# Kernel optimization log

Measured on AMD Instinct MI355X. Metric: run time of the kernel, lower is better.

## Reference

```python
import jax, jax.numpy as jnp
import numpy as np

# ---- static config (mirrors ProposalLayerModule param) ----
FEAT_STRIDE = 16
PRE_NMS_TOPN = 6000
POST_NMS_TOPN = 300
NMS_THRESH = 0.7
MIN_SIZE = 16.0
NUM_ANCHORS = 9


def _generate_anchors():
    """Replicates generate_anchors(base_size=16, ratios=[0.5,1,2], scales=[8,16,32])."""
    base = np.array([0.0, 0.0, 15.0, 15.0])
    ratios = np.array([0.5, 1.0, 2.0])
    scales = np.array([8.0, 16.0, 32.0])
    w = base[2] - base[0] + 1.0
    h = base[3] - base[1] + 1.0
    xc = base[0] + 0.5 * (w - 1.0)
    yc = base[1] + 0.5 * (h - 1.0)
    size = w * h
    ws = np.round(np.sqrt(size / ratios))
    hs = np.round(ws * ratios)
    ratio_anchors = np.stack([xc - 0.5 * (ws - 1), yc - 0.5 * (hs - 1),
                              xc + 0.5 * (ws - 1), yc + 0.5 * (hs - 1)], axis=1)
    out = []
    for a in ratio_anchors:
        aw = a[2] - a[0] + 1.0
        ah = a[3] - a[1] + 1.0
        axc = a[0] + 0.5 * (aw - 1.0)
        ayc = a[1] + 0.5 * (ah - 1.0)
        ws2 = aw * scales
        hs2 = ah * scales
        out.append(np.stack([axc - 0.5 * (ws2 - 1), ayc - 0.5 * (hs2 - 1),
                             axc + 0.5 * (ws2 - 1), ayc + 0.5 * (hs2 - 1)], axis=1))
    return np.concatenate(out, axis=0).astype(np.float32)  # (9, 4)

_ANCHORS = _generate_anchors()


def _nms_keep(iou, valid, thresh):
    """Greedy NMS over score-sorted boxes. Returns boolean keep mask."""
    n = iou.shape[0]
    idx = jnp.arange(n)
    def body(i, keep):
        sup = keep[i] & (iou[i] > thresh) & (idx > i)
        return keep & jnp.logical_not(sup)
    return jax.lax.fori_loop(0, n, body, valid)


def setup_inputs() -> dict:
    key = jax.random.key(0)
    k1, k2 = jax.random.split(key)
    H, W = 128, 192
    scores = jax.random.normal(k1, (1, 2 * NUM_ANCHORS, H, W), dtype=jnp.float32)
    # small deltas so exp(dw), exp(dh) stay in a realistic range
    bbox_deltas = jax.random.normal(k2, (1, 4 * NUM_ANCHORS, H, W), dtype=jnp.float32) * 0.1
    im_info = jnp.array([H * FEAT_STRIDE, W * FEAT_STRIDE, 1.0], dtype=jnp.float32)
    return {"scores": scores, "bbox_deltas": bbox_deltas, "im_info": im_info}


def reference(scores, bbox_deltas, im_info):
    A = NUM_ANCHORS
    s = scores[0, A:]                      # (A, H, W) fg scores
    Hf, Wf = s.shape[1], s.shape[2]
    # shifts, matching torch.meshgrid default indexing='ij' (x-major flatten)
    shift_x = jnp.arange(Wf, dtype=jnp.float32) * FEAT_STRIDE
    shift_y = jnp.arange(Hf, dtype=jnp.float32) * FEAT_STRIDE
    sx, sy = jnp.meshgrid(shift_x, shift_y, indexing='ij')   # (W, H)
    shifts = jnp.stack([sx.ravel(), sy.ravel(), sx.ravel(), sy.ravel()], axis=1)  # (K,4)
    anchors = (jnp.asarray(_ANCHORS)[None, :, :] + shifts[:, None, :]).reshape(-1, 4)  # (K*A,4)

    deltas = jnp.transpose(bbox_deltas[0], (1, 2, 0)).reshape(-1, 4)  # (H*W*A,4)
    sc = jnp.transpose(s, (1, 2, 0)).reshape(-1)                      # (H*W*A,)

    # bbox_transform_inv
    widths = anchors[:, 2] - anchors[:, 0] + 1.0
    heights = anchors[:, 3] - anchors[:, 1] + 1.0
    ctr_x = anchors[:, 0] + 0.5 * widths
    ctr_y = anchors[:, 1] + 0.5 * heights
    dx, dy, dw, dh = deltas[:, 0], deltas[:, 1], deltas[:, 2], deltas[:, 3]
    pcx = dx * widths + ctr_x
    pcy = dy * heights + ctr_y
    pw = jnp.exp(dw) * widths
    ph = jnp.exp(dh) * heights
    x1 = pcx - 0.5 * pw
    y1 = pcy - 0.5 * ph
    x2 = pcx + 0.5 * pw
    y2 = pcy + 0.5 * ph

    # clip_boxes
    x1 = jnp.clip(x1, 0.0, im_info[1] - 1.0)
    x2 = jnp.clip(x2, 0.0, im_info[1] - 1.0)
    y1 = jnp.clip(y1, 0.0, im_info[0] - 1.0)
    y2 = jnp.clip(y2, 0.0, im_info[0] - 1.0)
    boxes = jnp.stack([x1, y1, x2, y2], axis=1)

    # _filter_boxes (as a mask, jit-friendly)
    ms = MIN_SIZE * im_info[2]
    valid = ((x2 - x1 + 1.0) >= ms) & ((y2 - y1 + 1.0) >= ms)
    masked_sc = jnp.where(valid, sc, -jnp.inf)

    # sort by score descending + pre_nms_topN
    top_s, top_i = jax.lax.top_k(masked_sc, PRE_NMS_TOPN)
    b = boxes[top_i]                       # (PRE, 4), score-sorted
    vld = jnp.isfinite(top_s)

    # torchvision-style IoU (no +1) + greedy NMS
    area = (b[:, 2] - b[:, 0]) * (b[:, 3] - b[:, 1])
    ix1 = jnp.maximum(b[:, None, 0], b[None, :, 0])
    iy1 = jnp.maximum(b[:, None, 1], b[None, :, 1])
    ix2 = jnp.minimum(b[:, None, 2], b[None, :, 2])
    iy2 = jnp.minimum(b[:, None, 3], b[None, :, 3])
    inter = jnp.clip(ix2 - ix1, 0.0) * jnp.clip(iy2 - iy1, 0.0)
    iou = inter / jnp.maximum(area[:, None] + area[None, :] - inter, 1e-9)
    keep = _nms_keep(iou, vld, NMS_THRESH)

    # first post_nms_topN kept boxes (fixed-size, zero-padded), prepend batch idx 0
    cum = jnp.cumsum(keep.astype(jnp.int32))
    pos = jnp.where(keep & (cum <= POST_NMS_TOPN), cum - 1, POST_NMS_TOPN)
    rows = jnp.concatenate([jnp.zeros((PRE_NMS_TOPN, 1), jnp.float32), b], axis=1)
    out = jnp.zeros((POST_NMS_TOPN + 1, 5), jnp.float32).at[pos].set(rows)[:POST_NMS_TOPN]
    return out
```

## Files before the change

### kernel.cpp

```cpp
#include <hip/hip_runtime.h>

#define NCELL 24576
#define NTOT  221184
#define NBIN13 8192
#define TOPN  6000
#define POSTN 300
#define NPADR 6016
#define NW    94
#define CW    8
#define NCHUNK 12
#define NCB   16
#define SLOT  1024
#define CAP2  (NCB*SLOT)

__global__ void decode_kernel(const float* __restrict__ scores,
                              const float* __restrict__ deltas,
                              const float* __restrict__ iminfo,
                              float4* __restrict__ boxes,
                              unsigned* __restrict__ skeys,
                              unsigned short* __restrict__ skeys16) {
#pragma clang fp contract(off)
    int c = blockIdx.x * blockDim.x + threadIdx.x;
    if (c >= NCELL) return;
    const float AW[9] = {184.f,368.f,736.f,128.f,256.f,512.f, 88.f,176.f,352.f};
    const float AH[9] = { 96.f,192.f,384.f,128.f,256.f,512.f,176.f,352.f,704.f};
    float sx = (float)((c >> 7) << 4);
    float sy = (float)((c & 127) << 4);
    float imh = iminfo[0], imw = iminfo[1], ims = iminfo[2];
    float xhi = imw - 1.0f, yhi = imh - 1.0f;
    float ms = 16.0f * ims;
    float ctrx = sx + 8.0f, ctry = sy + 8.0f;
    const float* sbase = scores + 9 * NCELL + c;
    const float* dbase = deltas + c;
#pragma unroll
    for (int a = 0; a < 9; ++a) {
        float sc = sbase[a * NCELL];
        float dx = dbase[(4 * a + 0) * NCELL];
        float dy = dbase[(4 * a + 1) * NCELL];
        float dw = dbase[(4 * a + 2) * NCELL];
        float dh = dbase[(4 * a + 3) * NCELL];
        float pcx = dx * AW[a] + ctrx;
        float pcy = dy * AH[a] + ctry;
        float pw = expf(dw) * AW[a];
        float ph = expf(dh) * AH[a];
        float x1 = pcx - 0.5f * pw;
        float y1 = pcy - 0.5f * ph;
        float x2 = pcx + 0.5f * pw;
        float y2 = pcy + 0.5f * ph;
        x1 = fminf(fmaxf(x1, 0.0f), xhi);
        x2 = fminf(fmaxf(x2, 0.0f), xhi);
        y1 = fminf(fmaxf(y1, 0.0f), yhi);
        y2 = fminf(fmaxf(y2, 0.0f), yhi);
        bool valid = ((x2 - x1 + 1.0f) >= ms) && ((y2 - y1 + 1.0f) >= ms);
        unsigned u = __float_as_uint(sc);
        unsigned key = (u & 0x80000000u) ? ~u : (u | 0x80000000u);
        if (!valid) key = 0x007FFFFFu;
        boxes[a * NCELL + c] = make_float4(x1, y1, x2, y2);
        skeys[a * NCELL + c] = key;
        skeys16[a * NCELL + c] = (unsigned short)(key >> 16);
    }
}

__global__ __launch_bounds__(1024) void compactT_kernel(const unsigned* __restrict__ skeys,
                                                        const unsigned short* __restrict__ skeys16,
                                                        unsigned* __restrict__ meta16,
                                                        unsigned long long* __restrict__ cbuf) {
    __shared__ unsigned hist[NBIN13];
    __shared__ unsigned psum[1024];
    __shared__ unsigned csum[256];
    __shared__ unsigned sB, sAbove, sT, sCount;
    int tid = threadIdx.x, bid = blockIdx.x;
    for (int b = tid; b < NBIN13; b += 1024) hist[b] = 0u;
    if (tid == 0) sCount = 0u;
    __syncthreads();
    const uint4* s16 = (const uint4*)skeys16;
    for (int q = tid; q < NTOT / 8; q += 1024) {
        uint4 u = s16[q];
        atomicAdd(&hist[(u.x & 0xFFFFu) >> 3], 1u);
        atomicAdd(&hist[u.x >> 19], 1u);
        atomicAdd(&hist[(u.y & 0xFFFFu) >> 3], 1u);
        atomicAdd(&hist[u.y >> 19], 1u);
        atomicAdd(&hist[(u.z & 0xFFFFu) >> 3], 1u);
        atomicAdd(&hist[u.z >> 19], 1u);
        atomicAdd(&hist[(u.w & 0xFFFFu) >> 3], 1u);
        atomicAdd(&hist[u.w >> 19], 1u);
    }
    __syncthreads();
    unsigned s = 0;
#pragma unroll
    for (int q = 0; q < 8; ++q) s += hist[tid * 8 + q];
    psum[tid] = s;
    __syncthreads();
    if (tid < 256)
        csum[tid] = psum[tid * 4] + psum[tid * 4 + 1] + psum[tid * 4 + 2] + psum[tid * 4 + 3];
    __syncthreads();
    if (tid < 64) {
        int lane = tid;
        unsigned c0 = csum[lane * 4 + 0], c1 = csum[lane * 4 + 1];
        unsigned c2 = csum[lane * 4 + 2], c3 = csum[lane * 4 + 3];
        unsigned ls = c0 + c1 + c2 + c3;
        unsigned v = ls;
#pragma unroll
        for (int o = 1; o < 64; o <<= 1) {
            unsigned t = __shfl_down(v, o, 64);
            if (lane + o < 64) v += t;
        }
        unsigned sufExcl = v - ls;
        unsigned a3 = sufExcl;
        unsigned a2 = a3 + c3;
        unsigned a1 = a2 + c2;
        unsigned a0 = a1 + c1;
        if (a0 < TOPN && a0 + c0 >= TOPN) { sB = lane * 4 + 0; sAbove = a0; }
        if (a1 < TOPN && a1 + c1 >= TOPN) { sB = lane * 4 + 1; sAbove = a1; }
        if (a2 < TOPN && a2 + c2 >= TOPN) { sB = lane * 4 + 2; sAbove = a2; }
        if (a3 < TOPN && a3 + c3 >= TOPN) { sB = lane * 4 + 3; sAbove = a3; }
    }
    __syncthreads();
    if (tid < 32) {
        unsigned B = sB, above = sAbove;
        unsigned h = hist[B * 32 + tid];
        unsigned v = h;
#pragma unroll
        for (int o = 1; o < 32; o <<= 1) {
            unsigned t = __shfl_down(v, o, 64);
            if (tid + o < 32) v += t;
        }
        unsigned sufExcl = v - h;
        unsigned ab = above + sufExcl;
        if (ab < TOPN && ab + h >= TOPN) sT = B * 32 + tid;
    }
    __syncthreads();
    unsigned T = sT;
    int base = bid * (NTOT / NCB);
    const uint4* s4b = (const uint4*)(skeys + base);
    for (int q = tid; q < (NTOT / NCB) / 4; q += 1024) {
        uint4 u = s4b[q];
        unsigned k4[4] = {u.x, u.y, u.z, u.w};
#pragma unroll
        for (int k = 0; k < 4; ++k) {
            if ((k4[k] >> 19) >= T) {
                unsigned lp = atomicAdd(&sCount, 1u);
                if (lp < SLOT) {
                    int m = base + 4 * q + k;
                    unsigned n = (unsigned)((m % NCELL) * 9 + (m / NCELL));
                    cbuf[(bid << 10) + lp] =
                        ((unsigned long long)k4[k] << 32) | (unsigned long long)(~n);
                }
            }
        }
    }
    __syncthreads();
    unsigned cnt = sCount; if (cnt > SLOT) cnt = SLOT;
    for (int e = cnt + tid; e < SLOT; e += 1024) cbuf[(bid << 10) + e] = 0ULL;
    if (tid == 0) meta16[bid] = cnt;
}

__global__ __launch_bounds__(256) void rankscatter_kernel(const unsigned long long* __restrict__ cbuf,
                                                          const unsigned* __restrict__ meta16,
                                                          const float4* __restrict__ boxes,
                                                          float4* __restrict__ sortedbox) {
    __shared__ unsigned long long jk[512];
    __shared__ unsigned scnt[NCB];
    int tid = threadIdx.x;
    if (tid < NCB) scnt[tid] = meta16[tid];
    __syncthreads();
    int i = blockIdx.x * 32 + (tid >> 3);
    int slice = tid & 7;
    unsigned long long ki = cbuf[i];
    unsigned cr = 0;
    for (int jt = 0; jt < CAP2 / 512; ++jt) {
        int b = jt >> 1;
        unsigned cb = scnt[b];
        if ((jt & 1) ? (cb <= 512u) : (cb == 0u)) continue;
        __syncthreads();
        for (int q = tid; q < 512; q += 256) jk[q] = cbuf[(jt << 9) + q];
        __syncthreads();
#pragma unroll 8
        for (int j = 0; j < 64; ++j) cr += (jk[slice + (j << 3)] > ki) ? 1u : 0u;
    }
    cr += __shfl_down(cr, 4, 8);
    cr += __shfl_down(cr, 2, 8);
    cr += __shfl_down(cr, 1, 8);
    if (slice == 0 && ki != 0ULL && cr < NPADR) {
        unsigned n = ~(unsigned)ki;
        unsigned m = (n % 9u) * (unsigned)NCELL + (n / 9u);
        sortedbox[cr] = boxes[m];
    }
}

__global__ __launch_bounds__(256) void matrix_kernel(const float4* __restrict__ sortedbox,
                                                     unsigned long long* __restrict__ rowr,
                                                     unsigned long long* __restrict__ diagw,
                                                     unsigned long long* __restrict__ diagT) {
#pragma clang fp contract(off)
    __shared__ float4 jb[256];
    __shared__ float  ja[256];
    int tid = threadIdx.x;
    int lane = tid & 63, wave = tid >> 6;
    int i0 = blockIdx.y << 6;
    int i = i0 + lane;
    int w = (blockIdx.x << 2) + wave;
    int jbase = blockIdx.x << 8;
    unsigned long long word = 0ULL;

    if (jbase + 255 > i0) {
        int jg = jbase + tid;
        float4 v = (jg < NPADR) ? sortedbox[jg] : make_float4(0.f, 0.f, 0.f, 0.f);
        jb[tid] = v;
        ja[tid] = (v.z - v.x) * (v.w - v.y);
        __syncthreads();
        if (w < NW && ((w << 6) + 63) > i) {
            float4 bi = sortedbox[i];
            float ai = (bi.z - bi.x) * (bi.w - bi.y);
            int jl0 = wave << 6;
            int jg0 = (w << 6);
#pragma unroll 8
            for (int j = 0; j < 64; ++j) {
                float4 bj = jb[jl0 + j];
                float aj = ja[jl0 + j];
                float iw = fminf(bi.z, bj.z) - fmaxf(bi.x, bj.x);
                float ih = fminf(bi.w, bj.w) - fmaxf(bi.y, bj.y);
                iw = fmaxf(iw, 0.0f);
                ih = fmaxf(ih, 0.0f);
                float inter = iw * ih;
                float denom = fmaxf(ai + aj - inter, 1e-9f);
                bool sup = (jg0 + j > i) && (inter / denom > 0.7f);
                word |= (unsigned long long)sup << j;
            }
        }
    }
    if (w < NW) {
        if (w >= (i >> 6))
            rowr[(size_t)i * NW + w] = word;
        if ((i >> 9) == (w >> 3) && w >= (i >> 6)) {
            unsigned long long col = 0ULL;
#pragma unroll
            for (int jbit = 0; jbit < 64; ++jbit) {
                unsigned long long m = __ballot((word >> jbit) & 1ULL);
                if (lane == jbit) col = m;
            }
            if (w == (i >> 6))
                diagT[((size_t)w << 6) + lane] = col;
            else
                diagw[((size_t)w << 9) + (i & 511)] = col;
        }
    }
}

__global__ __launch_bounds__(512) void scan_kernel(const unsigned long long* __restrict__ rowr,
                                                   const unsigned long long* __restrict__ diagw,
                                                   const unsigned long long* __restrict__ diagT,
                                                   const float4* __restrict__ sortedbox,
                                                   float* __restrict__ out) {
    __shared__ __align__(16) unsigned long long cblk[2][CW * 512];
    __shared__ __align__(16) unsigned long long ldsT[2][CW * 64];
    __shared__ unsigned long long gm[128];
    __shared__ int keptArr[POSTN];
    __shared__ int s_kept, s_done;
    int tid = threadIdx.x;
    int lane = tid & 63, wave = tid >> 6;

    if (tid < 128) gm[tid] = (tid == 93) ? ~((1ULL << 48) - 1) : 0ULL;
    if (tid == 0) { s_kept = 0; s_done = 0; }
    for (int pe = tid; pe < CW * 256; pe += 512) {
        int q = pe >> 8, r = (pe & 255) << 1;
        if (q > (r >> 6))
            *(ulonglong2*)&cblk[0][(q << 9) + r] =
                *(const ulonglong2*)&diagw[((size_t)q << 9) + r];
    }
    for (int pe = tid; pe < CW * 32; pe += 512) {
        int e = pe << 1;
        *(ulonglong2*)&ldsT[0][e] = *(const ulonglong2*)&diagT[e];
    }
    __syncthreads();

    int kA = 0;
    int kB = 0;
    for (int c = 0; c < NCHUNK; ++c) {
        int buf = c & 1, nbuf = buf ^ 1;
        int wbase = c * CW;
        if (wave == 0) {
            unsigned long long dgT[CW];
            unsigned long long gml[CW];
#pragma unroll
            for (int q = 0; q < CW; ++q) dgT[q] = ldsT[buf][(q << 6) + lane];
#pragma unroll
            for (int q = 0; q < CW; ++q) gml[q] = (wbase + q < NW) ? gm[wbase + q] : ~0ULL;
            unsigned long long lowmask = (1ULL << lane) - 1ULL;
            unsigned chunk_sup = 0;
            int kept = kB;
            int done = 0;
            int qmax = (NW - wbase < CW) ? (NW - wbase) : CW;
            for (int q = 0; q < qmax; ++q) {
                unsigned long long csup = __ballot((chunk_sup >> q) & 1u);
                unsigned long long live = ~(gml[q] | csup);
                if (wbase + q == NW - 1) live &= (1ULL << 48) - 1;
                if (!live) continue;
                bool alive = (live >> lane) & 1ULL;
                unsigned long long x = live;
                for (;;) {
                    bool sup = (dgT[q] & x & lowmask) != 0ULL;
                    unsigned long long xn = __ballot(alive && !sup);
                    if (xn == x) break;
                    x = xn;
                }
                unsigned long long kb = x;
                if (kb) {
                    int nk = __popcll(kb);
                    int myr = __popcll(kb & lowmask);
                    if (((kb >> lane) & 1ULL) && (kept + myr < POSTN))
                        keptArr[kept + myr] = ((wbase + q) << 6) + lane;
                    kept += nk;
                    if (kept >= POSTN) { kept = POSTN; done = 1; break; }
                    if (q < CW - 1) {
                        unsigned long long pr[CW];
#pragma unroll
                        for (int t = 0; t < CW; ++t)
                            pr[t] = cblk[buf][(t << 9) + (q << 6) + lane];
#pragma unroll
                        for (int t = 0; t < CW; ++t)
                            if (t > q && (pr[t] & kb)) chunk_sup |= 1u << t;
                    }
                }
            }
            if (lane == 0) { s_kept = kept; s_done = done; }
        } else {
            int t = tid - 64;
            if (c + 1 < NCHUNK) {
                int wb2 = wbase + CW;
                for (int pe = t; pe < CW * 256; pe += 448) {
                    int q = pe >> 8, r = (pe & 255) << 1;
                    if (q > (r >> 6)) {
                        ulonglong2 v = make_ulonglong2(0ULL, 0ULL);
                        if (wb2 + q < NW && wb2 + (r >> 6) < NW)
                            v = *(const ulonglong2*)&diagw[((size_t)(wb2 + q) << 9) + r];
                        *(ulonglong2*)&cblk[nbuf][(q << 9) + r] = v;
                    }
                }
                for (int pe = t; pe < CW * 32; pe += 448) {
                    int e = pe << 1, q = e >> 6;
                    ulonglong2 v = make_ulonglong2(0ULL, 0ULL);
                    if (wb2 + q < NW) v = *(const ulonglong2*)&diagT[((size_t)wb2 << 6) + e];
                    *(ulonglong2*)&ldsT[nbuf][e] = v;
                }
            }
            {
                int w2 = wbase + CW;
                int nw2 = NW - w2;
                int nr2 = kB - kA;
                if (c > 0 && nr2 > 0 && nw2 > 0) {
                    int npair = nw2 >> 1;
                    int tot = nr2 * npair;
                    for (int idx = t; idx < tot; idx += 448) {
                        int s = idx / npair, po = idx - s * npair;
                        int row = keptArr[kA + s];
                        ulonglong2 v = *(const ulonglong2*)&rowr[(size_t)row * NW + w2 + (po << 1)];
                        if (v.x) atomicOr(&gm[w2 + (po << 1)], v.x);
                        if (v.y) atomicOr(&gm[w2 + (po << 1) + 1], v.y);
                    }
                }
            }
        }
        __syncthreads();
        int keptNow = s_kept;
        bool fin = (s_done != 0) || (c == NCHUNK - 1);
        if (!fin && keptNow > kB) {
            int w1 = wbase + CW;
            int nw1 = NW - w1; if (nw1 > CW) nw1 = CW;
            int npair1 = nw1 >> 1;
            int po = tid & 3;
            for (int s = kB + (tid >> 2); s < keptNow; s += 128) {
                if (po < npair1) {
                    int row = keptArr[s];
                    ulonglong2 v = *(const ulonglong2*)&rowr[(size_t)row * NW + w1 + (po << 1)];
                    if (v.x) atomicOr(&gm[w1 + (po << 1)], v.x);
                    if (v.y) atomicOr(&gm[w1 + (po << 1) + 1], v.y);
                }
            }
        }
        kA = kB;
        kB = keptNow;
        if (fin) break;
        __syncthreads();
    }
    __syncthreads();

    int kept = s_kept;
    for (int k = tid; k < POSTN; k += 512) {
        float4 bb = make_float4(0.f, 0.f, 0.f, 0.f);
        if (k < kept) bb = sortedbox[keptArr[k]];
        out[k * 5 + 0] = 0.0f;
        out[k * 5 + 1] = bb.x;
        out[k * 5 + 2] = bb.y;
        out[k * 5 + 3] = bb.z;
        out[k * 5 + 4] = bb.w;
    }
}

extern "C" void kernel_launch(void* const* d_in, const int* in_sizes, int n_in,
                              void* d_out, int out_size, void* d_ws, size_t ws_size,
                              hipStream_t stream) {
    const float* scores = (const float*)d_in[0];
    const float* deltas = (const float*)d_in[1];
    const float* iminfo = (const float*)d_in[2];
    char* w = (char*)d_ws;
    float4*   boxes = (float4*)w;
    unsigned* skeys = (unsigned*)(w + 3538944);
    unsigned long long* rowr = (unsigned long long*)w;
    unsigned* meta16 = (unsigned*)(w + 4786176);
    unsigned long long* cbuf = (unsigned long long*)(w + 4786240);
    float4* sortedbox = (float4*)(w + 4917312);
    unsigned long long* diagw = (unsigned long long*)(w + 5013568);
    unsigned long long* diagT = (unsigned long long*)(w + 5398592);
    unsigned short* skeys16 = (unsigned short*)(w + 5446720);
    float* out = (float*)d_out;

    decode_kernel<<<NCELL / 256, 256, 0, stream>>>(scores, deltas, iminfo, boxes, skeys, skeys16);
    compactT_kernel<<<NCB, 1024, 0, stream>>>(skeys, skeys16, meta16, cbuf);
    rankscatter_kernel<<<CAP2 / 32, 256, 0, stream>>>(cbuf, meta16, boxes, sortedbox);
    matrix_kernel<<<dim3(24, 94), 256, 0, stream>>>(sortedbox, rowr, diagw, diagT);
    scan_kernel<<<1, 512, 0, stream>>>(rowr, diagw, diagT, sortedbox, out);
}
```

Baseline: 148.6 us.

## Fuse score histogram into decode kernel via shared-memory and global atomics

The 13-bit score-key histogram is now built inside the decode kernel. Each block accumulates a local shared-memory histogram and flushes the non-zero bins to a global histogram with atomics. The compaction kernel then just copies the global histogram, instead of each of its 16 blocks redundantly rereading all 16-bit keys and re-histogramming them. This drops the skeys16 buffer and a large redundant pass, at the cost of a memset, per-block histogram init and flush (8192 bins for 96 blocks), and global atomic traffic.

```diff
diff --git a/kernel.cpp b/kernel.cpp
--- a/kernel.cpp
+++ b/kernel.cpp
@@ -18,51 +18,61 @@
                               const float* __restrict__ iminfo,
                               float4* __restrict__ boxes,
                               unsigned* __restrict__ skeys,
-                              unsigned short* __restrict__ skeys16) {
+                              unsigned* __restrict__ ghist) {
 #pragma clang fp contract(off)
-    int c = blockIdx.x * blockDim.x + threadIdx.x;
-    if (c >= NCELL) return;
-    const float AW[9] = {184.f,368.f,736.f,128.f,256.f,512.f, 88.f,176.f,352.f};
-    const float AH[9] = { 96.f,192.f,384.f,128.f,256.f,512.f,176.f,352.f,704.f};
-    float sx = (float)((c >> 7) << 4);
-    float sy = (float)((c & 127) << 4);
-    float imh = iminfo[0], imw = iminfo[1], ims = iminfo[2];
-    float xhi = imw - 1.0f, yhi = imh - 1.0f;
-    float ms = 16.0f * ims;
-    float ctrx = sx + 8.0f, ctry = sy + 8.0f;
-    const float* sbase = scores + 9 * NCELL + c;
-    const float* dbase = deltas + c;
-#pragma unroll
-    for (int a = 0; a < 9; ++a) {
-        float sc = sbase[a * NCELL];
-        float dx = dbase[(4 * a + 0) * NCELL];
-        float dy = dbase[(4 * a + 1) * NCELL];
-        float dw = dbase[(4 * a + 2) * NCELL];
-        float dh = dbase[(4 * a + 3) * NCELL];
-        float pcx = dx * AW[a] + ctrx;
-        float pcy = dy * AH[a] + ctry;
-        float pw = expf(dw) * AW[a];
-        float ph = expf(dh) * AH[a];
-        float x1 = pcx - 0.5f * pw;
-        float y1 = pcy - 0.5f * ph;
-        float x2 = pcx + 0.5f * pw;
-        float y2 = pcy + 0.5f * ph;
-        x1 = fminf(fmaxf(x1, 0.0f), xhi);
-        x2 = fminf(fmaxf(x2, 0.0f), xhi);
-        y1 = fminf(fmaxf(y1, 0.0f), yhi);
-        y2 = fminf(fmaxf(y2, 0.0f), yhi);
-        bool valid = ((x2 - x1 + 1.0f) >= ms) && ((y2 - y1 + 1.0f) >= ms);
-        unsigned u = __float_as_uint(sc);
-        unsigned key = (u & 0x80000000u) ? ~u : (u | 0x80000000u);
-        if (!valid) key = 0x007FFFFFu;
-        boxes[a * NCELL + c] = make_float4(x1, y1, x2, y2);
-        skeys[a * NCELL + c] = key;
-        skeys16[a * NCELL + c] = (unsigned short)(key >> 16);
+    __shared__ unsigned lhist[NBIN13];
+    int tid = threadIdx.x;
+    for (int b = tid; b < NBIN13; b += 256) lhist[b] = 0u;
+    __syncthreads();
+    int c = blockIdx.x * blockDim.x + tid;
+    if (c < NCELL) {
+        const float AW[9] = {184.f,368.f,736.f,128.f,256.f,512.f, 88.f,176.f,352.f};
+        const float AH[9] = { 96.f,192.f,384.f,128.f,256.f,512.f,176.f,352.f,704.f};
+        float sx = (float)((c >> 7) << 4);
+        float sy = (float)((c & 127) << 4);
+        float imh = iminfo[0], imw = iminfo[1], ims = iminfo[2];
+        float xhi = imw - 1.0f, yhi = imh - 1.0f;
+        float ms = 16.0f * ims;
+        float ctrx = sx + 8.0f, ctry = sy + 8.0f;
+        const float* sbase = scores + 9 * NCELL + c;
+        const float* dbase = deltas + c;
+#pragma unroll
+        for (int a = 0; a < 9; ++a) {
+            float sc = sbase[a * NCELL];
+            float dx = dbase[(4 * a + 0) * NCELL];
+            float dy = dbase[(4 * a + 1) * NCELL];
+            float dw = dbase[(4 * a + 2) * NCELL];
+            float dh = dbase[(4 * a + 3) * NCELL];
+            float pcx = dx * AW[a] + ctrx;
+            float pcy = dy * AH[a] + ctry;
+            float pw = expf(dw) * AW[a];
+            float ph = expf(dh) * AH[a];
+            float x1 = pcx - 0.5f * pw;
+            float y1 = pcy - 0.5f * ph;
+            float x2 = pcx + 0.5f * pw;
+            float y2 = pcy + 0.5f * ph;
+            x1 = fminf(fmaxf(x1, 0.0f), xhi);
+            x2 = fminf(fmaxf(x2, 0.0f), xhi);
+            y1 = fminf(fmaxf(y1, 0.0f), yhi);
+            y2 = fminf(fmaxf(y2, 0.0f), yhi);
+            bool valid = ((x2 - x1 + 1.0f) >= ms) && ((y2 - y1 + 1.0f) >= ms);
+            unsigned u = __float_as_uint(sc);
+            unsigned key = (u & 0x80000000u) ? ~u : (u | 0x80000000u);
+            if (!valid) key = 0x007FFFFFu;
+            boxes[a * NCELL + c] = make_float4(x1, y1, x2, y2);
+            skeys[a * NCELL + c] = key;
+            atomicAdd(&lhist[key >> 19], 1u);
+        }
+    }
+    __syncthreads();
+    for (int b = tid; b < NBIN13; b += 256) {
+        unsigned v = lhist[b];
+        if (v) atomicAdd(&ghist[b], v);
     }
 }
 
 __global__ __launch_bounds__(1024) void compactT_kernel(const unsigned* __restrict__ skeys,
-                                                        const unsigned short* __restrict__ skeys16,
+                                                        const unsigned* __restrict__ ghist,
                                                         unsigned* __restrict__ meta16,
                                                         unsigned long long* __restrict__ cbuf) {
     __shared__ unsigned hist[NBIN13];
@@ -70,21 +80,12 @@
     __shared__ unsigned csum[256];
     __shared__ unsigned sB, sAbove, sT, sCount;
     int tid = threadIdx.x, bid = blockIdx.x;
-    for (int b = tid; b < NBIN13; b += 1024) hist[b] = 0u;
+    {
+        const uint4* gh4 = (const uint4*)ghist;
+        uint4* h4 = (uint4*)hist;
+        for (int q = tid; q < NBIN13 / 4; q += 1024) h4[q] = gh4[q];
+    }
     if (tid == 0) sCount = 0u;
-    __syncthreads();
-    const uint4* s16 = (const uint4*)skeys16;
-    for (int q = tid; q < NTOT / 8; q += 1024) {
-        uint4 u = s16[q];
-        atomicAdd(&hist[(u.x & 0xFFFFu) >> 3], 1u);
-        atomicAdd(&hist[u.x >> 19], 1u);
-        atomicAdd(&hist[(u.y & 0xFFFFu) >> 3], 1u);
-        atomicAdd(&hist[u.y >> 19], 1u);
-        atomicAdd(&hist[(u.z & 0xFFFFu) >> 3], 1u);
-        atomicAdd(&hist[u.z >> 19], 1u);
-        atomicAdd(&hist[(u.w & 0xFFFFu) >> 3], 1u);
-        atomicAdd(&hist[u.w >> 19], 1u);
-    }
     __syncthreads();
     unsigned s = 0;
 #pragma unroll
@@ -412,11 +413,12 @@
     float4* sortedbox = (float4*)(w + 4917312);
     unsigned long long* diagw = (unsigned long long*)(w + 5013568);
     unsigned long long* diagT = (unsigned long long*)(w + 5398592);
-    unsigned short* skeys16 = (unsigned short*)(w + 5446720);
+    unsigned* ghist = (unsigned*)(w + 5446720);
     float* out = (float*)d_out;
 
-    decode_kernel<<<NCELL / 256, 256, 0, stream>>>(scores, deltas, iminfo, boxes, skeys, skeys16);
-    compactT_kernel<<<NCB, 1024, 0, stream>>>(skeys, skeys16, meta16, cbuf);
+    hipMemsetAsync(ghist, 0, NBIN13 * sizeof(unsigned), stream);
+    decode_kernel<<<NCELL / 256, 256, 0, stream>>>(scores, deltas, iminfo, boxes, skeys, ghist);
+    compactT_kernel<<<NCB, 1024, 0, stream>>>(skeys, ghist, meta16, cbuf);
     rankscatter_kernel<<<CAP2 / 32, 256, 0, stream>>>(cbuf, meta16, boxes, sortedbox);
     matrix_kernel<<<dim3(24, 94), 256, 0, stream>>>(sortedbox, rowr, diagw, diagT);
     scan_kernel<<<1, 512, 0, stream>>>(rowr, diagw, diagT, sortedbox, out);
```

New measurement: 135.7 us. 1.1x faster.
